# Performance work log

Measured on AMD Instinct MI355X. Metric: run time of the kernel, lower is better.

The kernel has to match this reference:

```python
import jax, jax.numpy as jnp
import numpy as np

N_NODES = 50000
N_EDGES = 800000
D_IN = 64
D_OUT = 64


def setup_inputs() -> dict:
    key = jax.random.key(0)
    k1, k2, k3, k4 = jax.random.split(key, 4)
    x = jax.random.normal(k1, (N_NODES, D_IN), dtype=jnp.float32)
    edge_index = jax.random.randint(k2, (2, N_EDGES), 0, N_NODES, dtype=jnp.int64)
    scale = np.sqrt(1.0 / D_IN).astype(np.float32)
    W_msg = jax.random.normal(k3, (D_OUT, D_IN), dtype=jnp.float32) * scale
    W_self = jax.random.normal(k4, (D_OUT, D_IN), dtype=jnp.float32) * scale
    b_msg = jnp.zeros((D_OUT,), dtype=jnp.float32)
    b_self = jnp.zeros((D_OUT,), dtype=jnp.float32)
    return {"x": x, "edge_index": edge_index, "W_msg": W_msg, "b_msg": b_msg,
            "W_self": W_self, "b_self": b_self}


def reference(x, edge_index, W_msg, b_msg, W_self, b_self):
    row, col = edge_index[0], edge_index[1]
    n = x.shape[0]
    # message projection on all source nodes, then gather per edge
    msgs_src = x @ W_msg.T + b_msg            # [N, D_OUT]
    per_edge = msgs_src[row]                  # [E, D_OUT] gather
    # scatter-mean into destination nodes
    summed = jax.ops.segment_sum(per_edge, col, num_segments=n)          # [N, D_OUT]
    counts = jax.ops.segment_sum(jnp.ones_like(col, dtype=x.dtype), col,
                                 num_segments=n)                         # [N]
    agg = summed / jnp.maximum(counts, 1.0)[:, None]
    self_out = x @ W_self.T + b_self
    return self_out + agg
```

## Files before the change

kernel.cpp:

```cpp
#include <hip/hip_runtime.h>

constexpr int N_NODES = 50000;
constexpr int N_EDGES = 800000;
constexpr int D = 64;
constexpr int NB = (N_NODES + 63) / 64;
constexpr int BUCKET_CAP = 1280;

typedef __attribute__((ext_vector_type(8))) short short8;
typedef __attribute__((ext_vector_type(4))) float f32x4;

static __device__ inline unsigned short f2bf(float f) {
    unsigned u = __float_as_uint(f);
    unsigned r = (u + 0x7FFFu + ((u >> 16) & 1u)) >> 16;
    return (unsigned short)r;
}
static __device__ inline unsigned pack2(float lo, float hi) {
    return (unsigned)f2bf(lo) | ((unsigned)f2bf(hi) << 16);
}
static __device__ inline float bf2f(unsigned short b) {
    return __uint_as_float((unsigned)b << 16);
}

constexpr int BIN_BLOCKS = 256;
constexpr int EDGES_PER_BIN_BLOCK = (N_EDGES + BIN_BLOCKS - 1) / BIN_BLOCKS;

__global__ __launch_bounds__(512) void k_bin_place(
    const float* __restrict__ x, unsigned short* __restrict__ xb,
    const float* __restrict__ W_msg, const float* __restrict__ W_self,
    unsigned short* __restrict__ B_packed,
    const int* __restrict__ edge_index,
    unsigned* __restrict__ g_cursor, unsigned* __restrict__ bucket_data)
{
    __shared__ unsigned ent_sh[EDGES_PER_BIN_BLOCK];
    __shared__ unsigned lcount[NB];
    __shared__ unsigned lbase[NB];

    int tid = threadIdx.x;

    for (int b = tid; b < NB; b += 512) lcount[b] = 0u;

    int gid = blockIdx.x * 512 + tid;
    for (int t = gid; t < N_NODES * D / 4; t += BIN_BLOCKS * 512) {
        float4 v = ((const float4*)x)[t];
        uint2 p;
        p.x = pack2(v.x, v.y);
        p.y = pack2(v.z, v.w);
        ((uint2*)xb)[t] = p;
    }
    if (blockIdx.x == 0) {
        for (int idx = tid; idx < 64 * 128; idx += 512) {
            int n = idx >> 7;
            int k = idx & 127;
            float v = (k < 64) ? W_self[n * 64 + k] : W_msg[n * 64 + (k - 64)];
            B_packed[idx] = f2bf(v);
        }
    }

    int e0 = blockIdx.x * EDGES_PER_BIN_BLOCK;
    int e1 = min(e0 + EDGES_PER_BIN_BLOCK, N_EDGES);
    int ne = e1 - e0;
    __syncthreads();

    for (int e = e0 + tid; e < e1; e += 512) {
        int dst = edge_index[N_EDGES + e];
        int src = edge_index[e];
        ent_sh[e - e0] = ((unsigned)src << 16) | (unsigned)dst;
        atomicAdd(&lcount[dst >> 6], 1u);
    }
    __syncthreads();

    for (int b = tid; b < NB; b += 512) {
        unsigned c = lcount[b];
        lbase[b] = c ? ((unsigned)b * BUCKET_CAP + atomicAdd(&g_cursor[b], c)) : 0u;
    }
    __syncthreads();
    for (int b = tid; b < NB; b += 512) lcount[b] = 0u;
    __syncthreads();

    for (int i = tid; i < ne; i += 512) {
        unsigned ent = ent_sh[i];
        unsigned dst = ent & 0xFFFFu;
        unsigned b   = dst >> 6;
        unsigned off = atomicAdd(&lcount[b], 1u);
        bucket_data[lbase[b] + off] = (ent >> 16) | ((dst & 63u) << 16);
    }
}

constexpr int A_STRIDE = 136;

__global__ __launch_bounds__(512) void k_fused(
    const unsigned short* __restrict__ x_bf16,
    const unsigned short* __restrict__ B_packed,
    const float* __restrict__ b_msg, const float* __restrict__ b_self,
    const unsigned* __restrict__ cursor,
    const unsigned* __restrict__ bucket_data,
    float* __restrict__ out)
{
    __shared__ __align__(16) unsigned short A_sh[64 * A_STRIDE];
    __shared__ __align__(16) unsigned short B_sh[64 * A_STRIDE];
    __shared__ unsigned short sorted_sh[BUCKET_CAP];
    __shared__ unsigned cnt_sh[64];
    __shared__ unsigned off_sh[64];
    __shared__ unsigned woff_sh[64];

    int tid  = threadIdx.x;
    int w    = tid >> 6;
    int lane = tid & 63;
    int r0   = blockIdx.x * 64;

    unsigned start = (unsigned)blockIdx.x * BUCKET_CAP;
    unsigned end   = start + cursor[blockIdx.x];

    if (tid < 64) cnt_sh[tid] = 0u;
    for (int idx = tid; idx < 64 * 8; idx += 512) {
        int row = idx >> 3;
        int c   = idx & 7;
        int g   = r0 + row;
        uint4 v = make_uint4(0u, 0u, 0u, 0u);
        if (g < N_NODES) v = *(const uint4*)&x_bf16[g * D + c * 8];
        *(uint4*)&A_sh[row * A_STRIDE + c * 8] = v;
    }
    for (int idx = tid; idx < 64 * 16; idx += 512) {
        int n = idx >> 4;
        int c = idx & 15;
        uint4 v = *(const uint4*)&B_packed[n * 128 + c * 8];
        *(uint4*)&B_sh[n * A_STRIDE + c * 8] = v;
    }
    __syncthreads();

    for (unsigned i = start + tid; i < end; i += 512u)
        atomicAdd(&cnt_sh[bucket_data[i] >> 16], 1u);
    __syncthreads();

    if (tid < 64) {
        unsigned c = cnt_sh[tid];
        unsigned xsum = c;
        #pragma unroll
        for (int s = 1; s < 64; s <<= 1) {
            unsigned v = (unsigned)__shfl_up((int)xsum, s);
            if (lane >= s) xsum += v;
        }
        off_sh[tid]  = xsum - c;
        woff_sh[tid] = xsum - c;
    }
    __syncthreads();

    for (unsigned i = start + tid; i < end; i += 512u) {
        unsigned e = bucket_data[i];
        unsigned slot = atomicAdd(&woff_sh[e >> 16], 1u);
        sorted_sh[slot] = (unsigned short)(e & 0xFFFFu);
    }
    __syncthreads();

    int Q = lane >> 4;
    int f = lane & 15;

    for (int i = 0; i < 8; ++i) {
        int lrow = w * 8 + i;
        unsigned s0 = off_sh[lrow];
        unsigned dc = cnt_sh[lrow];
        unsigned e_end = s0 + dc;

        float a0 = 0.f, a1 = 0.f, a2 = 0.f, a3 = 0.f;
        for (unsigned b = s0; b < e_end; b += 16u) {
            unsigned ii[4];
            ushort4  rv[4];
            #pragma unroll
            for (int u = 0; u < 4; ++u) {
                ii[u] = b + 4u * u + (unsigned)Q;
                unsigned src = (ii[u] < e_end) ? (unsigned)sorted_sh[ii[u]] : 0u;
                rv[u] = *(const ushort4*)&x_bf16[(src << 6) + 4u * (unsigned)f];
            }
            #pragma unroll
            for (int u = 0; u < 4; ++u) {
                if (ii[u] < e_end) {
                    a0 += bf2f(rv[u].x); a1 += bf2f(rv[u].y);
                    a2 += bf2f(rv[u].z); a3 += bf2f(rv[u].w);
                }
            }
        }
        a0 += __shfl_xor(a0, 16); a1 += __shfl_xor(a1, 16);
        a2 += __shfl_xor(a2, 16); a3 += __shfl_xor(a3, 16);
        a0 += __shfl_xor(a0, 32); a1 += __shfl_xor(a1, 32);
        a2 += __shfl_xor(a2, 32); a3 += __shfl_xor(a3, 32);

        if (Q == 0) {
            float inv = dc ? 1.0f / (float)dc : 0.0f;
            uint2 p;
            p.x = pack2(a0 * inv, a1 * inv);
            p.y = pack2(a2 * inv, a3 * inv);
            *(uint2*)&A_sh[lrow * A_STRIDE + 64 + 4 * f] = p;
        }
    }
    __syncthreads();

    int wm   = w & 3;
    int ng   = (w >> 2) * 2;
    int quad = lane >> 4;
    int l15  = lane & 15;

    f32x4 accr[2] = {{0.f,0.f,0.f,0.f},{0.f,0.f,0.f,0.f}};

    #pragma unroll
    for (int k0 = 0; k0 < 128; k0 += 32) {
        short8 a = *(const short8*)&A_sh[(16 * wm + l15) * A_STRIDE + k0 + quad * 8];
        #pragma unroll
        for (int t = 0; t < 2; ++t) {
            short8 b = *(const short8*)&B_sh[(16 * (ng + t) + l15) * A_STRIDE + k0 + quad * 8];
            accr[t] = __builtin_amdgcn_mfma_f32_16x16x32_bf16(a, b, accr[t], 0, 0, 0);
        }
    }

    #pragma unroll
    for (int t = 0; t < 2; ++t) {
        int col = (ng + t) * 16 + l15;
        float bs = b_self[col];
        float bm = b_msg[col];
        #pragma unroll
        for (int r = 0; r < 4; ++r) {
            int lrow = 16 * wm + quad * 4 + r;
            int grow = r0 + lrow;
            if (grow < N_NODES) {
                float vv = accr[t][r] + bs + (cnt_sh[lrow] > 0u ? bm : 0.0f);
                out[grow * D + col] = vv;
            }
        }
    }
}

extern "C" void kernel_launch(void* const* d_in, const int* in_sizes, int n_in,
                              void* d_out, int out_size, void* d_ws, size_t ws_size,
                              hipStream_t stream) {
    const float* x      = (const float*)d_in[0];
    const int*   edges  = (const int*)  d_in[1];
    const float* W_msg  = (const float*)d_in[2];
    const float* b_msg  = (const float*)d_in[3];
    const float* W_self = (const float*)d_in[4];
    const float* b_self = (const float*)d_in[5];
    float*       out    = (float*)d_out;

    char* ws = (char*)d_ws;
    unsigned*       cursor      = (unsigned*)(ws + 0);
    unsigned short* B_packed    = (unsigned short*)(ws + 4096);
    unsigned*       bucket_data = (unsigned*)(ws + 20480);
    unsigned short* x_bf16      = (unsigned short*)(ws + 4030464);

    hipMemsetAsync(cursor, 0, NB * sizeof(unsigned), stream);

    k_bin_place<<<BIN_BLOCKS, 512, 0, stream>>>(x, x_bf16, W_msg, W_self,
                                                B_packed, edges, cursor, bucket_data);
    k_fused<<<NB, 512, 0, stream>>>(x_bf16, B_packed, b_msg, b_self,
                                    cursor, bucket_data, out);
}
```

Measured before the change: 116.4 us.

## Pad per-row edge lists to multiples of four with a zero row, one row per quarter-wave

Each quarter-wave now handles its own destination row, so the cross-lane shuffle reduction goes away and every row runs through its own loop instead of eight serial rows per wave. Edge lists are padded to multiples of four with pointers to an appended all-zero bf16 row, which removes the per-element bounds checks. The bucket capacity grows to make room for the padding, which moves the x_bf16 workspace offset and increases LDS use. Load imbalance between the four rows a wave handles at once can leave lanes idle, since each pass waits for the longest row.

```diff
diff --git a/kernel.cpp b/kernel.cpp
--- a/kernel.cpp
+++ b/kernel.cpp
@@ -4,7 +4,8 @@
 constexpr int N_EDGES = 800000;
 constexpr int D = 64;
 constexpr int NB = (N_NODES + 63) / 64;
-constexpr int BUCKET_CAP = 1280;
+constexpr int BUCKET_CAP = 1536;
+constexpr unsigned ZERO_ROW = 50000u;
 
 typedef __attribute__((ext_vector_type(8))) short short8;
 typedef __attribute__((ext_vector_type(4))) float f32x4;
@@ -54,6 +55,9 @@
             float v = (k < 64) ? W_self[n * 64 + k] : W_msg[n * 64 + (k - 64)];
             B_packed[idx] = f2bf(v);
         }
+    } else if (blockIdx.x == 1) {
+        if (tid < 8)
+            *(uint4*)&xb[ZERO_ROW * D + tid * 8] = make_uint4(0u, 0u, 0u, 0u);
     }
 
     int e0 = blockIdx.x * EDGES_PER_BIN_BLOCK;
@@ -100,7 +104,7 @@
     __shared__ __align__(16) unsigned short B_sh[64 * A_STRIDE];
     __shared__ unsigned short sorted_sh[BUCKET_CAP];
     __shared__ unsigned cnt_sh[64];
-    __shared__ unsigned off_sh[64];
+    __shared__ unsigned poff_sh[64];
     __shared__ unsigned woff_sh[64];
 
     int tid  = threadIdx.x;
@@ -126,6 +130,8 @@
         uint4 v = *(const uint4*)&B_packed[n * 128 + c * 8];
         *(uint4*)&B_sh[n * A_STRIDE + c * 8] = v;
     }
+    for (int i = tid; i < BUCKET_CAP; i += 512)
+        sorted_sh[i] = (unsigned short)ZERO_ROW;
     __syncthreads();
 
     for (unsigned i = start + tid; i < end; i += 512u)
@@ -133,15 +139,16 @@
     __syncthreads();
 
     if (tid < 64) {
-        unsigned c = cnt_sh[tid];
-        unsigned xsum = c;
+        unsigned c  = cnt_sh[tid];
+        unsigned pc = (c + 3u) & ~3u;
+        unsigned xsum = pc;
         #pragma unroll
         for (int s = 1; s < 64; s <<= 1) {
             unsigned v = (unsigned)__shfl_up((int)xsum, s);
             if (lane >= s) xsum += v;
         }
-        off_sh[tid]  = xsum - c;
-        woff_sh[tid] = xsum - c;
+        poff_sh[tid] = xsum - pc;
+        woff_sh[tid] = xsum - pc;
     }
     __syncthreads();
 
@@ -155,42 +162,32 @@
     int Q = lane >> 4;
     int f = lane & 15;
 
-    for (int i = 0; i < 8; ++i) {
-        int lrow = w * 8 + i;
-        unsigned s0 = off_sh[lrow];
+    #pragma unroll
+    for (int pass = 0; pass < 2; ++pass) {
+        int lrow = w * 8 + pass * 4 + Q;
+        unsigned s0 = poff_sh[lrow];
         unsigned dc = cnt_sh[lrow];
-        unsigned e_end = s0 + dc;
+        unsigned pc = (dc + 3u) & ~3u;
 
         float a0 = 0.f, a1 = 0.f, a2 = 0.f, a3 = 0.f;
-        for (unsigned b = s0; b < e_end; b += 16u) {
-            unsigned ii[4];
-            ushort4  rv[4];
+        for (unsigned j = 0; j < pc; j += 4u) {
+            ushort4 rv[4];
             #pragma unroll
             for (int u = 0; u < 4; ++u) {
-                ii[u] = b + 4u * u + (unsigned)Q;
-                unsigned src = (ii[u] < e_end) ? (unsigned)sorted_sh[ii[u]] : 0u;
+                unsigned src = (unsigned)sorted_sh[s0 + j + u];
                 rv[u] = *(const ushort4*)&x_bf16[(src << 6) + 4u * (unsigned)f];
             }
             #pragma unroll
             for (int u = 0; u < 4; ++u) {
-                if (ii[u] < e_end) {
-                    a0 += bf2f(rv[u].x); a1 += bf2f(rv[u].y);
-                    a2 += bf2f(rv[u].z); a3 += bf2f(rv[u].w);
-                }
+                a0 += bf2f(rv[u].x); a1 += bf2f(rv[u].y);
+                a2 += bf2f(rv[u].z); a3 += bf2f(rv[u].w);
             }
         }
-        a0 += __shfl_xor(a0, 16); a1 += __shfl_xor(a1, 16);
-        a2 += __shfl_xor(a2, 16); a3 += __shfl_xor(a3, 16);
-        a0 += __shfl_xor(a0, 32); a1 += __shfl_xor(a1, 32);
-        a2 += __shfl_xor(a2, 32); a3 += __shfl_xor(a3, 32);
-
-        if (Q == 0) {
-            float inv = dc ? 1.0f / (float)dc : 0.0f;
-            uint2 p;
-            p.x = pack2(a0 * inv, a1 * inv);
-            p.y = pack2(a2 * inv, a3 * inv);
-            *(uint2*)&A_sh[lrow * A_STRIDE + 64 + 4 * f] = p;
-        }
+        float inv = dc ? 1.0f / (float)dc : 0.0f;
+        uint2 p;
+        p.x = pack2(a0 * inv, a1 * inv);
+        p.y = pack2(a2 * inv, a3 * inv);
+        *(uint2*)&A_sh[lrow * A_STRIDE + 64 + 4 * f] = p;
     }
     __syncthreads();
 
@@ -243,7 +240,7 @@
     unsigned*       cursor      = (unsigned*)(ws + 0);
     unsigned short* B_packed    = (unsigned short*)(ws + 4096);
     unsigned*       bucket_data = (unsigned*)(ws + 20480);
-    unsigned short* x_bf16      = (unsigned short*)(ws + 4030464);
+    unsigned short* x_bf16      = (unsigned short*)(ws + 20480 + (size_t)NB * BUCKET_CAP * 4);
 
     hipMemsetAsync(cursor, 0, NB * sizeof(unsigned), stream);
 
```

Measured after the change: 112.9 us. -3.0%, faster.
